# Performance work log

Hardware: AMD Instinct MI355X
Metric: run time of the kernel (lower is better)

Reference implementation:

```python
import math
import jax, jax.numpy as jnp
import numpy as np
from jax import lax

B = 4; N = 4096; F = 15; A = 24          # batch, tcr_num, feature_num, aa_num
HID = 10; H = 1; HD = 10; AFN = 14       # attn hidden, heads, head dim, sum(filter_num)
KS = [2, 3, 4, 5, 6, 7]; FN = [3, 3, 3, 2, 2, 1]
K = int(N * 0.05)                        # routing topk = 204
SCALE = np.float32(1.0 / math.sqrt(HD))


def setup_inputs() -> dict:
    key = jax.random.key(0)
    ks = jax.random.split(key, 24)
    inp = {"x": jax.random.normal(ks[0], (B, N, F, A), jnp.float32)}
    for i, (h, f) in enumerate(zip(KS, FN)):
        inp["conv_w%d" % h] = jax.random.normal(ks[1 + 2 * i], (f, F, h), jnp.float32) * 0.1
        inp["conv_b%d" % h] = jax.random.normal(ks[2 + 2 * i], (f,), jnp.float32) * 0.1
    specs = [("q", HID, AFN), ("k", HID, AFN), ("v", HID, AFN), ("attn", AFN, HID), ("mil", 2, AFN)]
    for j, (nm, o, i_) in enumerate(specs):
        inp["w_" + nm] = jax.random.normal(ks[13 + 2 * j], (o, i_), jnp.float32) * 0.1
        inp["b_" + nm] = jax.random.normal(ks[14 + 2 * j], (o,), jnp.float32) * 0.1
    return inp


def reference(x, conv_w2, conv_b2, conv_w3, conv_b3, conv_w4, conv_b4,
              conv_w5, conv_b5, conv_w6, conv_b6, conv_w7, conv_b7,
              w_q, b_q, w_k, b_k, w_v, b_v, w_attn, b_attn, w_mil, b_mil):
    # --- per-sequence conv feature extraction ---
    xc = x.reshape(-1, F, A)  # [B*N, 15, 24]
    feats = []
    for w, b in [(conv_w2, conv_b2), (conv_w3, conv_b3), (conv_w4, conv_b4),
                 (conv_w5, conv_b5), (conv_w6, conv_b6), (conv_w7, conv_b7)]:
        y = lax.conv_general_dilated(xc, w, (1,), 'VALID',
                                     dimension_numbers=('NCH', 'OIH', 'NCH'))
        y = jax.nn.relu(y + b[None, :, None])
        feats.append(jnp.max(y, axis=-1))  # AdaptiveMaxPool1d(1)
    out = jnp.concatenate(feats, axis=1).reshape(B, N, AFN)  # [B, N, 14]

    # --- QKV projections, split into heads -> [B, H, N, HD] ---
    q = (out @ w_q.T + b_q).reshape(B, N, H, HD).transpose(0, 2, 1, 3)
    k = (out @ w_k.T + b_k).reshape(B, N, H, HD).transpose(0, 2, 1, 3)
    v = (out @ w_v.T + b_v).reshape(B, N, H, HD).transpose(0, 2, 1, 3)

    # --- bi-level routing: full scores, topk over head-mean (detached in torch) ---
    scores_raw = jnp.einsum('bhnd,bhmd->bhnm', q, k)  # [B, H, N, N]
    a_r = jnp.mean(lax.stop_gradient(scores_raw), axis=1)  # [B, N, N]
    _, idx = lax.top_k(a_r, K)  # [B, N, K] int32
    idx_r = jnp.broadcast_to(idx[:, None], (B, H, N, K))

    scores = jnp.take_along_axis(scores_raw * SCALE, idx_r, axis=3)  # [B, H, N, K]
    # gather values per (batch, head, query): v_g[b,h,i,j] = v[b,h,idx[b,h,i,j]]
    v_g = jax.vmap(jax.vmap(lambda vh, ih: vh[ih]))(v, idx_r)  # [B, H, N, K, HD]

    probs = jax.nn.softmax(scores, axis=-1)  # dropout is identity at p=0 / eval
    ctx = jnp.einsum('bhnk,bhnkd->bhnd', probs, v_g)  # [B, H, N, HD]
    ctx = ctx.transpose(0, 2, 1, 3).reshape(B, N, HID)

    ctx = ctx @ w_attn.T + b_attn          # [B, N, 14]
    logits = ctx @ w_mil.T + b_mil          # [B, N, 2]
    pooled = jnp.sum(logits, axis=1) / N    # [B, 2]
    return pooled, probs[:, :, :, None, :]  # probs shaped [B, H, N, 1, K] as in torch
```

## Files before the change

kernel.cpp:

```cpp
#include <hip/hip_runtime.h>
#include <math.h>

#define NB 4
#define NN 4096
#define KSEL 204
#define NBINS 512
#define CANDN 256
#define QKSCALE 0.31622776601683794f

#define WS_Q 0
#define WS_KT (NB * NN * 10)
#define WS_V (2 * NB * NN * 10)
#define WS_LG (3 * NB * NN * 10)

#define SEQ_PER_BLOCK 16


__global__ __launch_bounds__(256) void featqkv_kernel(
    const float* __restrict__ x,
    const float* __restrict__ w2, const float* __restrict__ b2,
    const float* __restrict__ w3, const float* __restrict__ b3,
    const float* __restrict__ w4, const float* __restrict__ b4,
    const float* __restrict__ w5, const float* __restrict__ b5,
    const float* __restrict__ w6, const float* __restrict__ b6,
    const float* __restrict__ w7, const float* __restrict__ b7,
    const float* __restrict__ wq, const float* __restrict__ bq,
    const float* __restrict__ wk, const float* __restrict__ bk,
    const float* __restrict__ wv, const float* __restrict__ bv,
    float* __restrict__ q_out, float* __restrict__ kT_out, float* __restrict__ v_out)
{
    __shared__ __align__(16) float xs[SEQ_PER_BLOCK * 360];
    __shared__ float wpad[14 * 105];
    __shared__ float bconv[14];
    __shared__ float wqkv[420];
    __shared__ float bqkv[30];
    __shared__ float feats[SEQ_PER_BLOCK * 14];

    const int t = threadIdx.x;
    const int g0 = blockIdx.x * SEQ_PER_BLOCK;

    {
        const float4* xg4 = reinterpret_cast<const float4*>(x + (size_t)g0 * 360);
        float4* xs4 = reinterpret_cast<float4*>(xs);
        for (int i = t; i < SEQ_PER_BLOCK * 90; i += 256) xs4[i] = xg4[i];
    }

    for (int i = t; i < 14 * 105; i += 256) {
        const int ch = i / 105;
        const int r = i - ch * 105;
        const int c = r / 7;
        const int j = r - (r / 7) * 7;
        float val = 0.f;
        if (ch < 3)       { if (j < 2) val = w2[ch * 30 + c * 2 + j]; }
        else if (ch < 6)  { if (j < 3) val = w3[(ch - 3) * 45 + c * 3 + j]; }
        else if (ch < 9)  { if (j < 4) val = w4[(ch - 6) * 60 + c * 4 + j]; }
        else if (ch < 11) { if (j < 5) val = w5[(ch - 9) * 75 + c * 5 + j]; }
        else if (ch < 13) { if (j < 6) val = w6[(ch - 11) * 90 + c * 6 + j]; }
        else              { val = w7[c * 7 + j]; }
        wpad[i] = val;
    }
    if (t < 3) bconv[t] = b2[t];
    else if (t < 6) bconv[t] = b3[t - 3];
    else if (t < 9) bconv[t] = b4[t - 6];
    else if (t < 11) bconv[t] = b5[t - 9];
    else if (t < 13) bconv[t] = b6[t - 11];
    else if (t == 13) bconv[t] = b7[0];
    for (int i = t; i < 140; i += 256) wqkv[i] = wq[i];
    for (int i = t; i < 140; i += 256) wqkv[140 + i] = wk[i];
    for (int i = t; i < 140; i += 256) wqkv[280 + i] = wv[i];
    if (t < 10) bqkv[t] = bq[t];
    else if (t < 20) bqkv[t] = bk[t - 10];
    else if (t < 30) bqkv[t] = bv[t - 20];
    __syncthreads();

    const int seq = t >> 4;
    const int wkr = t & 15;

    if (wkr < 14) {
        const int ch = wkr;
        int T;
        if (ch < 3) T = 23; else if (ch < 6) T = 22; else if (ch < 9) T = 21;
        else if (ch < 11) T = 20; else if (ch < 13) T = 19; else T = 18;

        float acc[23];
#pragma unroll
        for (int u = 0; u < 23; u++) acc[u] = 0.f;
        const float* xrow = &xs[seq * 360];
        const float* wrow = &wpad[ch * 105];
        for (int c = 0; c < 15; c++) {
            float xr[30];
            const float4* xp = reinterpret_cast<const float4*>(xrow + c * 24);
#pragma unroll
            for (int u4 = 0; u4 < 6; u4++) {
                const float4 xv = xp[u4];
                xr[u4 * 4 + 0] = xv.x; xr[u4 * 4 + 1] = xv.y;
                xr[u4 * 4 + 2] = xv.z; xr[u4 * 4 + 3] = xv.w;
            }
#pragma unroll
            for (int u = 24; u < 30; u++) xr[u] = 0.f;
#pragma unroll
            for (int j = 0; j < 7; j++) {
                const float wv_ = wrow[c * 7 + j];
#pragma unroll
                for (int tt = 0; tt < 23; tt++)
                    acc[tt] = fmaf(xr[tt + j], wv_, acc[tt]);
            }
        }
        float m = -3.0e38f;
#pragma unroll
        for (int tt = 0; tt < 23; tt++)
            if (tt < T) m = fmaxf(m, acc[tt]);
        feats[seq * 14 + ch] = fmaxf(m + bconv[ch], 0.f);
    }
    __syncthreads();

    const int g = g0 + seq;
    const int b_ = g >> 12;
    const int n_ = g & 4095;
    for (int o = wkr; o < 30; o += 16) {
        const int type = o / 10;
        const int comp = o % 10;
        const float* wrow = &wqkv[type * 140 + comp * 14];
        const float* frow = &feats[seq * 14];
        float a = bqkv[type * 10 + comp];
#pragma unroll
        for (int ii = 0; ii < 14; ii++) a = fmaf(frow[ii], wrow[ii], a);
        if (type == 0) q_out[(size_t)g * 10 + comp] = a;
        else if (type == 1)
            kT_out[(size_t)b_ * 40960 + (size_t)(n_ >> 6) * 640 + comp * 64 + (n_ & 63)] = a;
        else v_out[(size_t)g * 10 + comp] = a;
    }
}

__device__ __forceinline__ float dec_key(unsigned int k) {
    return (k & 0x80000000u) ? __uint_as_float(k ^ 0x80000000u)
                             : __uint_as_float(~k);
}
__device__ __forceinline__ unsigned int enc_key(float s) {
    unsigned int u = __float_as_uint(s);
    return (u & 0x80000000u) ? ~u : (u | 0x80000000u);
}

__global__ __launch_bounds__(256, 8) void attn_kernel(
    const float* __restrict__ qbuf, const float* __restrict__ kTbuf,
    const float* __restrict__ vbuf,
    const float* __restrict__ w_attn, const float* __restrict__ b_attn,
    const float* __restrict__ w_mil, const float* __restrict__ b_mil,
    float* __restrict__ out_probs, float* __restrict__ logits)
{
    __shared__ unsigned int base_[NBINS];
    __shared__ unsigned int bc_[NBINS];
    __shared__ unsigned long long cand[CANDN];
    __shared__ float hpart[4], lpart[4], fpart[4];
    __shared__ unsigned int wtot[4];
    __shared__ float ctxp[40];
    __shared__ float ctx_sh[10];
    __shared__ float attn_sh[14];

    const int t = threadIdx.x;
    const int lane = t & 63;
    const int w = t >> 6;
    const int row = blockIdx.x;
    const int b_ = row >> 12;

    float qr[10];
    {
        const float* qp = qbuf + (size_t)row * 10;
#pragma unroll
        for (int c = 0; c < 10; c++) qr[c] = qp[c];
    }
    const float* kTb = kTbuf + (size_t)b_ * 40960;
    float sc[16];
    float vhi = -1e30f, vlo = 1e30f;
#pragma unroll
    for (int i = 0; i < 4; i++) {
        const float4* kp = reinterpret_cast<const float4*>(
            kTb + (size_t)(i * 16 + (t >> 4)) * 640 + (t & 15) * 4);
        float ax = 0.f, ay = 0.f, az = 0.f, aw = 0.f;
#pragma unroll
        for (int c = 0; c < 10; c++) {
            const float4 kv = kp[c * 16];
            ax = fmaf(qr[c], kv.x, ax);
            ay = fmaf(qr[c], kv.y, ay);
            az = fmaf(qr[c], kv.z, az);
            aw = fmaf(qr[c], kv.w, aw);
        }
        sc[i * 4 + 0] = ax; sc[i * 4 + 1] = ay;
        sc[i * 4 + 2] = az; sc[i * 4 + 3] = aw;
        vhi = fmaxf(vhi, fmaxf(fmaxf(ax, ay), fmaxf(az, aw)));
        vlo = fminf(vlo, fminf(fminf(ax, ay), fminf(az, aw)));
    }
#pragma unroll
    for (int off = 32; off > 0; off >>= 1) {
        vhi = fmaxf(vhi, __shfl_xor(vhi, off));
        vlo = fminf(vlo, __shfl_xor(vlo, off));
    }
    if (lane == 0) { hpart[w] = vhi; lpart[w] = vlo; }
    base_[2 * t] = 0u; base_[2 * t + 1] = 0u;
    cand[t] = 0ULL;
    __syncthreads();
    const float hi = fmaxf(fmaxf(hpart[0], hpart[1]), fmaxf(hpart[2], hpart[3]));
    const float lo = fminf(fminf(lpart[0], lpart[1]), fminf(lpart[2], lpart[3]));
    const bool degen = (hi <= lo);

    float pv = 0.f;
    int jj = 0, p = KSEL;
    bool selected = false;
    const float smax = hi * QKSCALE;

    if (!degen) {
        const float scale = (float)(NBINS - 1) / (hi - lo);

#pragma unroll
        for (int i = 0; i < 16; i++) {
            const int bin = (int)fminf((sc[i] - lo) * scale, (float)(NBINS - 1));
            atomicAdd(&base_[bin], 1u);
        }
        __syncthreads();

        {
            const unsigned int c0 = base_[2 * t];
            const unsigned int c1 = base_[2 * t + 1];
            const unsigned int T_ = c0 + c1;
            unsigned int acc = T_;
#pragma unroll
            for (int off = 1; off < 64; off <<= 1) {
                unsigned int o = __shfl_down(acc, off);
                if (lane + off < 64) acc += o;
            }
            if (lane == 0) wtot[w] = acc;
            __syncthreads();
            unsigned int tail = 0u;
#pragma unroll
            for (int w2 = 1; w2 < 4; w2++) if (w2 > w) tail += wtot[w2];
            const unsigned int A = (acc - T_) + tail;
            base_[2 * t + 1] = A;
            base_[2 * t] = A + c1;
            bc_[2 * t + 1] = A;
            bc_[2 * t] = A + c1;
        }
        __syncthreads();

#pragma unroll
        for (int i = 0; i < 16; i++) {
            const int bin = (int)fminf((sc[i] - lo) * scale, (float)(NBINS - 1));
            const unsigned int bs = base_[bin];
            if (bs < KSEL) {
                const unsigned int pos = atomicAdd(&bc_[bin], 1u);
                if (pos < CANDN) {
                    const int j = (i >> 2) * 1024 + t * 4 + (i & 3);
                    cand[pos] = (((unsigned long long)enc_key(sc[i])) << 16)
                              | (unsigned long long)(4095 - j);
                }
            }
        }
        __syncthreads();

        const unsigned long long mine = cand[t];
        if (mine != 0ULL) {
            const float s = dec_key((unsigned int)(mine >> 16));
            const int bin = (int)fminf((s - lo) * scale, (float)(NBINS - 1));
            const unsigned int bs = base_[bin];
            unsigned int e2 = (bin > 0) ? base_[bin - 1] : 4096u;
            if (e2 > CANDN) e2 = CANDN;
            unsigned int rank = 0;
            for (unsigned int s2 = bs; s2 < e2; s2++)
                rank += (cand[s2] > mine) ? 1u : 0u;
            const unsigned int pp = bs + rank;
            if (pp < KSEL) {
                selected = true;
                p = (int)pp;
                jj = 4095 - (int)(mine & 0xFFFFu);
                pv = expf(s * QKSCALE - smax);
            }
        }
    } else {
        if (t < KSEL) {
            selected = true;
            p = t;
            jj = t;
            pv = 1.f;
        }
    }

    float dsum = pv;
#pragma unroll
    for (int off = 32; off > 0; off >>= 1) dsum += __shfl_xor(dsum, off);
    if (lane == 0) fpart[w] = dsum;
    __syncthreads();
    const float inv = 1.f / (fpart[0] + fpart[1] + fpart[2] + fpart[3]);

    float cx0 = 0.f, cx1 = 0.f, cx2 = 0.f, cx3 = 0.f, cx4 = 0.f;
    float cx5 = 0.f, cx6 = 0.f, cx7 = 0.f, cx8 = 0.f, cx9 = 0.f;
    if (selected) {
        const float pn = pv * inv;
        out_probs[(size_t)row * KSEL + p] = pn;
        const float* vr = vbuf + ((size_t)b_ * NN + (size_t)jj) * 10;
        const float2 v01 = reinterpret_cast<const float2*>(vr)[0];
        const float2 v23 = reinterpret_cast<const float2*>(vr)[1];
        const float2 v45 = reinterpret_cast<const float2*>(vr)[2];
        const float2 v67 = reinterpret_cast<const float2*>(vr)[3];
        const float2 v89 = reinterpret_cast<const float2*>(vr)[4];
        cx0 = pn * v01.x; cx1 = pn * v01.y;
        cx2 = pn * v23.x; cx3 = pn * v23.y;
        cx4 = pn * v45.x; cx5 = pn * v45.y;
        cx6 = pn * v67.x; cx7 = pn * v67.y;
        cx8 = pn * v89.x; cx9 = pn * v89.y;
    }
#pragma unroll
    for (int off = 32; off > 0; off >>= 1) {
        cx0 += __shfl_xor(cx0, off); cx1 += __shfl_xor(cx1, off);
        cx2 += __shfl_xor(cx2, off); cx3 += __shfl_xor(cx3, off);
        cx4 += __shfl_xor(cx4, off); cx5 += __shfl_xor(cx5, off);
        cx6 += __shfl_xor(cx6, off); cx7 += __shfl_xor(cx7, off);
        cx8 += __shfl_xor(cx8, off); cx9 += __shfl_xor(cx9, off);
    }
    if (lane == 0) {
        ctxp[w * 10 + 0] = cx0; ctxp[w * 10 + 1] = cx1; ctxp[w * 10 + 2] = cx2;
        ctxp[w * 10 + 3] = cx3; ctxp[w * 10 + 4] = cx4; ctxp[w * 10 + 5] = cx5;
        ctxp[w * 10 + 6] = cx6; ctxp[w * 10 + 7] = cx7; ctxp[w * 10 + 8] = cx8;
        ctxp[w * 10 + 9] = cx9;
    }
    __syncthreads();
    if (t < 10) ctx_sh[t] = ctxp[t] + ctxp[10 + t] + ctxp[20 + t] + ctxp[30 + t];
    __syncthreads();

    if (t < 14) {
        float a = b_attn[t];
#pragma unroll
        for (int d = 0; d < 10; d++) a = fmaf(ctx_sh[d], w_attn[t * 10 + d], a);
        attn_sh[t] = a;
    }
    __syncthreads();
    if (t < 2) {
        float lg = b_mil[t];
#pragma unroll
        for (int ii = 0; ii < 14; ii++) lg = fmaf(attn_sh[ii], w_mil[t * 14 + ii], lg);
        logits[(size_t)row * 2 + t] = lg;
    }
}

__global__ __launch_bounds__(256) void pool_kernel(
    const float* __restrict__ logits, float* __restrict__ out)
{
    __shared__ float red[256];
    const int t = threadIdx.x;
    const int bc = blockIdx.x;
    const int b_ = bc >> 1;
    const int c_ = bc & 1;
    float a = 0.f;
    for (int n2 = t; n2 < NN; n2 += 256)
        a += logits[((size_t)b_ * NN + n2) * 2 + c_];
    red[t] = a;
    __syncthreads();
    for (int off = 128; off > 0; off >>= 1) {
        if (t < off) red[t] += red[t + off];
        __syncthreads();
    }
    if (t == 0) out[bc] = red[0] * (1.f / 4096.f);
}

extern "C" void kernel_launch(void* const* d_in, const int* in_sizes, int n_in,
                              void* d_out, int out_size, void* d_ws, size_t ws_size,
                              hipStream_t stream) {
    const float* x  = (const float*)d_in[0];
    const float* w2 = (const float*)d_in[1];  const float* b2 = (const float*)d_in[2];
    const float* w3 = (const float*)d_in[3];  const float* b3 = (const float*)d_in[4];
    const float* w4 = (const float*)d_in[5];  const float* b4 = (const float*)d_in[6];
    const float* w5 = (const float*)d_in[7];  const float* b5 = (const float*)d_in[8];
    const float* w6 = (const float*)d_in[9];  const float* b6 = (const float*)d_in[10];
    const float* w7 = (const float*)d_in[11]; const float* b7 = (const float*)d_in[12];
    const float* wq = (const float*)d_in[13]; const float* bq = (const float*)d_in[14];
    const float* wk = (const float*)d_in[15]; const float* bk = (const float*)d_in[16];
    const float* wv = (const float*)d_in[17]; const float* bv = (const float*)d_in[18];
    const float* wat = (const float*)d_in[19]; const float* bat = (const float*)d_in[20];
    const float* wm = (const float*)d_in[21];  const float* bm = (const float*)d_in[22];

    float* ws = (float*)d_ws;
    float* qb = ws + WS_Q;
    float* kT = ws + WS_KT;
    float* vb = ws + WS_V;
    float* lg = ws + WS_LG;
    float* out = (float*)d_out;

    hipLaunchKernelGGL(featqkv_kernel, dim3(NB * NN / SEQ_PER_BLOCK), dim3(256), 0, stream,
                       x, w2, b2, w3, b3, w4, b4, w5, b5, w6, b6, w7, b7,
                       wq, bq, wk, bk, wv, bv, qb, kT, vb);
    hipLaunchKernelGGL(attn_kernel, dim3(NB * NN), dim3(256), 0, stream,
                       qb, kT, vb, wat, bat, wm, bm, out + 8, lg);
    hipLaunchKernelGGL(pool_kernel, dim3(8), dim3(256), 0, stream, lg, out);
}
```

Baseline: 320.1 us.

## Process two query rows per attention block and reuse each K load

Each attention block now handles two adjacent query rows, so every float4 of K is loaded once and used for both rows' dot products. All histogram, scan, candidate and softmax stages are interleaved across the two rows, which halves the grid and the number of barriers per row. K is also stored in a plain [batch, component, n] transposed layout so each thread reads contiguous float4s. In exchange it raises register and shared-memory use per block (launch bound lowered to 4) and gives fewer blocks for latency hiding.

```diff
diff --git a/kernel.cpp b/kernel.cpp
--- a/kernel.cpp
+++ b/kernel.cpp
@@ -126,8 +126,7 @@
 #pragma unroll
         for (int ii = 0; ii < 14; ii++) a = fmaf(frow[ii], wrow[ii], a);
         if (type == 0) q_out[(size_t)g * 10 + comp] = a;
-        else if (type == 1)
-            kT_out[(size_t)b_ * 40960 + (size_t)(n_ >> 6) * 640 + comp * 64 + (n_ & 63)] = a;
+        else if (type == 1) kT_out[((size_t)b_ * 10 + comp) * NN + n_] = a;
         else v_out[(size_t)g * 10 + comp] = a;
     }
 }
@@ -141,202 +140,276 @@
     return (u & 0x80000000u) ? ~u : (u | 0x80000000u);
 }
 
-__global__ __launch_bounds__(256, 8) void attn_kernel(
+__global__ __launch_bounds__(256, 4) void attn_kernel(
     const float* __restrict__ qbuf, const float* __restrict__ kTbuf,
     const float* __restrict__ vbuf,
     const float* __restrict__ w_attn, const float* __restrict__ b_attn,
     const float* __restrict__ w_mil, const float* __restrict__ b_mil,
     float* __restrict__ out_probs, float* __restrict__ logits)
 {
-    __shared__ unsigned int base_[NBINS];
-    __shared__ unsigned int bc_[NBINS];
-    __shared__ unsigned long long cand[CANDN];
-    __shared__ float hpart[4], lpart[4], fpart[4];
-    __shared__ unsigned int wtot[4];
-    __shared__ float ctxp[40];
-    __shared__ float ctx_sh[10];
-    __shared__ float attn_sh[14];
+    __shared__ unsigned int base_[2][NBINS];
+    __shared__ unsigned int bc_[2][NBINS];
+    __shared__ unsigned long long cand[2][CANDN];
+    __shared__ float hpart[2][4], lpart[2][4], fpart[2][4];
+    __shared__ unsigned int wtot[2][4];
+    __shared__ float ctxp[2][40];
+    __shared__ float ctx_sh[2][10];
+    __shared__ float attn_sh[2][14];
 
     const int t = threadIdx.x;
     const int lane = t & 63;
     const int w = t >> 6;
-    const int row = blockIdx.x;
-    const int b_ = row >> 12;
-
-    float qr[10];
+    const int r0 = blockIdx.x * 2;
+    const int b_ = r0 >> 12;
+
+    float qr[2][10];
     {
-        const float* qp = qbuf + (size_t)row * 10;
-#pragma unroll
-        for (int c = 0; c < 10; c++) qr[c] = qp[c];
-    }
-    const float* kTb = kTbuf + (size_t)b_ * 40960;
-    float sc[16];
-    float vhi = -1e30f, vlo = 1e30f;
+        const float4* qp4 = reinterpret_cast<const float4*>(qbuf + (size_t)r0 * 10);
+        const float4 a = qp4[0], b = qp4[1], c = qp4[2], d = qp4[3], e = qp4[4];
+        qr[0][0] = a.x; qr[0][1] = a.y; qr[0][2] = a.z; qr[0][3] = a.w;
+        qr[0][4] = b.x; qr[0][5] = b.y; qr[0][6] = b.z; qr[0][7] = b.w;
+        qr[0][8] = c.x; qr[0][9] = c.y;
+        qr[1][0] = c.z; qr[1][1] = c.w;
+        qr[1][2] = d.x; qr[1][3] = d.y; qr[1][4] = d.z; qr[1][5] = d.w;
+        qr[1][6] = e.x; qr[1][7] = e.y; qr[1][8] = e.z; qr[1][9] = e.w;
+    }
+    const float* kTb = kTbuf + (size_t)b_ * 10 * NN;
+    float sc[2][16];
+    float vhi[2], vlo[2];
+#pragma unroll
+    for (int rr = 0; rr < 2; rr++) { vhi[rr] = -1e30f; vlo[rr] = 1e30f; }
 #pragma unroll
     for (int i = 0; i < 4; i++) {
-        const float4* kp = reinterpret_cast<const float4*>(
-            kTb + (size_t)(i * 16 + (t >> 4)) * 640 + (t & 15) * 4);
-        float ax = 0.f, ay = 0.f, az = 0.f, aw = 0.f;
+        float a0x = 0.f, a0y = 0.f, a0z = 0.f, a0w = 0.f;
+        float a1x = 0.f, a1y = 0.f, a1z = 0.f, a1w = 0.f;
 #pragma unroll
         for (int c = 0; c < 10; c++) {
-            const float4 kv = kp[c * 16];
-            ax = fmaf(qr[c], kv.x, ax);
-            ay = fmaf(qr[c], kv.y, ay);
-            az = fmaf(qr[c], kv.z, az);
-            aw = fmaf(qr[c], kv.w, aw);
-        }
-        sc[i * 4 + 0] = ax; sc[i * 4 + 1] = ay;
-        sc[i * 4 + 2] = az; sc[i * 4 + 3] = aw;
-        vhi = fmaxf(vhi, fmaxf(fmaxf(ax, ay), fmaxf(az, aw)));
-        vlo = fminf(vlo, fminf(fminf(ax, ay), fminf(az, aw)));
+            const float4 kv = reinterpret_cast<const float4*>(kTb + c * NN)[i * 256 + t];
+            a0x = fmaf(qr[0][c], kv.x, a0x);
+            a0y = fmaf(qr[0][c], kv.y, a0y);
+            a0z = fmaf(qr[0][c], kv.z, a0z);
+            a0w = fmaf(qr[0][c], kv.w, a0w);
+            a1x = fmaf(qr[1][c], kv.x, a1x);
+            a1y = fmaf(qr[1][c], kv.y, a1y);
+            a1z = fmaf(qr[1][c], kv.z, a1z);
+            a1w = fmaf(qr[1][c], kv.w, a1w);
+        }
+        sc[0][i * 4 + 0] = a0x; sc[0][i * 4 + 1] = a0y;
+        sc[0][i * 4 + 2] = a0z; sc[0][i * 4 + 3] = a0w;
+        sc[1][i * 4 + 0] = a1x; sc[1][i * 4 + 1] = a1y;
+        sc[1][i * 4 + 2] = a1z; sc[1][i * 4 + 3] = a1w;
+        vhi[0] = fmaxf(vhi[0], fmaxf(fmaxf(a0x, a0y), fmaxf(a0z, a0w)));
+        vlo[0] = fminf(vlo[0], fminf(fminf(a0x, a0y), fminf(a0z, a0w)));
+        vhi[1] = fmaxf(vhi[1], fmaxf(fmaxf(a1x, a1y), fmaxf(a1z, a1w)));
+        vlo[1] = fminf(vlo[1], fminf(fminf(a1x, a1y), fminf(a1z, a1w)));
     }
 #pragma unroll
     for (int off = 32; off > 0; off >>= 1) {
-        vhi = fmaxf(vhi, __shfl_xor(vhi, off));
-        vlo = fminf(vlo, __shfl_xor(vlo, off));
-    }
-    if (lane == 0) { hpart[w] = vhi; lpart[w] = vlo; }
-    base_[2 * t] = 0u; base_[2 * t + 1] = 0u;
-    cand[t] = 0ULL;
-    __syncthreads();
-    const float hi = fmaxf(fmaxf(hpart[0], hpart[1]), fmaxf(hpart[2], hpart[3]));
-    const float lo = fminf(fminf(lpart[0], lpart[1]), fminf(lpart[2], lpart[3]));
-    const bool degen = (hi <= lo);
-
-    float pv = 0.f;
-    int jj = 0, p = KSEL;
-    bool selected = false;
-    const float smax = hi * QKSCALE;
-
-    if (!degen) {
-        const float scale = (float)(NBINS - 1) / (hi - lo);
-
-#pragma unroll
-        for (int i = 0; i < 16; i++) {
-            const int bin = (int)fminf((sc[i] - lo) * scale, (float)(NBINS - 1));
-            atomicAdd(&base_[bin], 1u);
-        }
-        __syncthreads();
-
-        {
-            const unsigned int c0 = base_[2 * t];
-            const unsigned int c1 = base_[2 * t + 1];
-            const unsigned int T_ = c0 + c1;
-            unsigned int acc = T_;
-#pragma unroll
-            for (int off = 1; off < 64; off <<= 1) {
-                unsigned int o = __shfl_down(acc, off);
-                if (lane + off < 64) acc += o;
+#pragma unroll
+        for (int rr = 0; rr < 2; rr++) {
+            vhi[rr] = fmaxf(vhi[rr], __shfl_xor(vhi[rr], off));
+            vlo[rr] = fminf(vlo[rr], __shfl_xor(vlo[rr], off));
+        }
+    }
+    if (lane == 0) {
+#pragma unroll
+        for (int rr = 0; rr < 2; rr++) { hpart[rr][w] = vhi[rr]; lpart[rr][w] = vlo[rr]; }
+    }
+    {
+        unsigned int* bz = &base_[0][0];
+#pragma unroll
+        for (int i = 0; i < 4; i++) bz[t + i * 256] = 0u;
+        unsigned long long* cz = &cand[0][0];
+        cz[t] = 0ULL; cz[t + 256] = 0ULL;
+    }
+    __syncthreads();
+
+    float hi[2], lo[2], scale[2], smax[2];
+    bool degen[2];
+#pragma unroll
+    for (int rr = 0; rr < 2; rr++) {
+        hi[rr] = fmaxf(fmaxf(hpart[rr][0], hpart[rr][1]), fmaxf(hpart[rr][2], hpart[rr][3]));
+        lo[rr] = fminf(fminf(lpart[rr][0], lpart[rr][1]), fminf(lpart[rr][2], lpart[rr][3]));
+        degen[rr] = (hi[rr] <= lo[rr]);
+        scale[rr] = degen[rr] ? 0.f : (float)(NBINS - 1) / (hi[rr] - lo[rr]);
+        smax[rr] = hi[rr] * QKSCALE;
+    }
+
+#pragma unroll
+    for (int rr = 0; rr < 2; rr++) {
+        if (!degen[rr]) {
+#pragma unroll
+            for (int i = 0; i < 16; i++) {
+                const int bin = (int)fminf((sc[rr][i] - lo[rr]) * scale[rr], (float)(NBINS - 1));
+                atomicAdd(&base_[rr][bin], 1u);
             }
-            if (lane == 0) wtot[w] = acc;
-            __syncthreads();
-            unsigned int tail = 0u;
-#pragma unroll
-            for (int w2 = 1; w2 < 4; w2++) if (w2 > w) tail += wtot[w2];
-            const unsigned int A = (acc - T_) + tail;
-            base_[2 * t + 1] = A;
-            base_[2 * t] = A + c1;
-            bc_[2 * t + 1] = A;
-            bc_[2 * t] = A + c1;
-        }
-        __syncthreads();
-
-#pragma unroll
-        for (int i = 0; i < 16; i++) {
-            const int bin = (int)fminf((sc[i] - lo) * scale, (float)(NBINS - 1));
-            const unsigned int bs = base_[bin];
-            if (bs < KSEL) {
-                const unsigned int pos = atomicAdd(&bc_[bin], 1u);
-                if (pos < CANDN) {
-                    const int j = (i >> 2) * 1024 + t * 4 + (i & 3);
-                    cand[pos] = (((unsigned long long)enc_key(sc[i])) << 16)
-                              | (unsigned long long)(4095 - j);
+        }
+    }
+    __syncthreads();
+
+    unsigned int c1s[2], Ts[2], accs[2];
+#pragma unroll
+    for (int rr = 0; rr < 2; rr++) {
+        const unsigned int c0 = base_[rr][2 * t];
+        const unsigned int c1 = base_[rr][2 * t + 1];
+        const unsigned int T_ = c0 + c1;
+        unsigned int acc = T_;
+#pragma unroll
+        for (int off = 1; off < 64; off <<= 1) {
+            unsigned int o = __shfl_down(acc, off);
+            if (lane + off < 64) acc += o;
+        }
+        if (lane == 0) wtot[rr][w] = acc;
+        c1s[rr] = c1; Ts[rr] = T_; accs[rr] = acc;
+    }
+    __syncthreads();
+#pragma unroll
+    for (int rr = 0; rr < 2; rr++) {
+        unsigned int tail = 0u;
+#pragma unroll
+        for (int w2 = 1; w2 < 4; w2++) if (w2 > w) tail += wtot[rr][w2];
+        const unsigned int A = (accs[rr] - Ts[rr]) + tail;
+        base_[rr][2 * t + 1] = A;
+        base_[rr][2 * t] = A + c1s[rr];
+        bc_[rr][2 * t + 1] = A;
+        bc_[rr][2 * t] = A + c1s[rr];
+    }
+    __syncthreads();
+
+#pragma unroll
+    for (int rr = 0; rr < 2; rr++) {
+        if (!degen[rr]) {
+#pragma unroll
+            for (int i = 0; i < 16; i++) {
+                const int bin = (int)fminf((sc[rr][i] - lo[rr]) * scale[rr], (float)(NBINS - 1));
+                const unsigned int bs = base_[rr][bin];
+                if (bs < KSEL) {
+                    const unsigned int pos = atomicAdd(&bc_[rr][bin], 1u);
+                    if (pos < CANDN) {
+                        const int j = (i >> 2) * 1024 + t * 4 + (i & 3);
+                        cand[rr][pos] = (((unsigned long long)enc_key(sc[rr][i])) << 16)
+                                      | (unsigned long long)(4095 - j);
+                    }
                 }
             }
         }
-        __syncthreads();
-
-        const unsigned long long mine = cand[t];
-        if (mine != 0ULL) {
-            const float s = dec_key((unsigned int)(mine >> 16));
-            const int bin = (int)fminf((s - lo) * scale, (float)(NBINS - 1));
-            const unsigned int bs = base_[bin];
-            unsigned int e2 = (bin > 0) ? base_[bin - 1] : 4096u;
-            if (e2 > CANDN) e2 = CANDN;
-            unsigned int rank = 0;
-            for (unsigned int s2 = bs; s2 < e2; s2++)
-                rank += (cand[s2] > mine) ? 1u : 0u;
-            const unsigned int pp = bs + rank;
-            if (pp < KSEL) {
-                selected = true;
-                p = (int)pp;
-                jj = 4095 - (int)(mine & 0xFFFFu);
-                pv = expf(s * QKSCALE - smax);
+    }
+    __syncthreads();
+
+    float pv[2]; int jj[2], p[2]; bool selected[2];
+#pragma unroll
+    for (int rr = 0; rr < 2; rr++) {
+        pv[rr] = 0.f; jj[rr] = 0; p[rr] = KSEL; selected[rr] = false;
+        if (!degen[rr]) {
+            const unsigned long long mine = cand[rr][t];
+            if (mine != 0ULL) {
+                const float s = dec_key((unsigned int)(mine >> 16));
+                const int bin = (int)fminf((s - lo[rr]) * scale[rr], (float)(NBINS - 1));
+                const unsigned int bs = base_[rr][bin];
+                unsigned int e2 = (bin > 0) ? base_[rr][bin - 1] : 4096u;
+                if (e2 > CANDN) e2 = CANDN;
+                unsigned int rank = 0;
+                for (unsigned int s2 = bs; s2 < e2; s2++)
+                    rank += (cand[rr][s2] > mine) ? 1u : 0u;
+                const unsigned int pp = bs + rank;
+                if (pp < KSEL) {
+                    selected[rr] = true;
+                    p[rr] = (int)pp;
+                    jj[rr] = 4095 - (int)(mine & 0xFFFFu);
+                    pv[rr] = expf(s * QKSCALE - smax[rr]);
+                }
             }
-        }
-    } else {
-        if (t < KSEL) {
-            selected = true;
-            p = t;
-            jj = t;
-            pv = 1.f;
-        }
-    }
-
-    float dsum = pv;
-#pragma unroll
-    for (int off = 32; off > 0; off >>= 1) dsum += __shfl_xor(dsum, off);
-    if (lane == 0) fpart[w] = dsum;
-    __syncthreads();
-    const float inv = 1.f / (fpart[0] + fpart[1] + fpart[2] + fpart[3]);
-
-    float cx0 = 0.f, cx1 = 0.f, cx2 = 0.f, cx3 = 0.f, cx4 = 0.f;
-    float cx5 = 0.f, cx6 = 0.f, cx7 = 0.f, cx8 = 0.f, cx9 = 0.f;
-    if (selected) {
-        const float pn = pv * inv;
-        out_probs[(size_t)row * KSEL + p] = pn;
-        const float* vr = vbuf + ((size_t)b_ * NN + (size_t)jj) * 10;
-        const float2 v01 = reinterpret_cast<const float2*>(vr)[0];
-        const float2 v23 = reinterpret_cast<const float2*>(vr)[1];
-        const float2 v45 = reinterpret_cast<const float2*>(vr)[2];
-        const float2 v67 = reinterpret_cast<const float2*>(vr)[3];
-        const float2 v89 = reinterpret_cast<const float2*>(vr)[4];
-        cx0 = pn * v01.x; cx1 = pn * v01.y;
-        cx2 = pn * v23.x; cx3 = pn * v23.y;
-        cx4 = pn * v45.x; cx5 = pn * v45.y;
-        cx6 = pn * v67.x; cx7 = pn * v67.y;
-        cx8 = pn * v89.x; cx9 = pn * v89.y;
-    }
+        } else {
+            if (t < KSEL) { selected[rr] = true; p[rr] = t; jj[rr] = t; pv[rr] = 1.f; }
+        }
+    }
+
+    float dsum[2];
+#pragma unroll
+    for (int rr = 0; rr < 2; rr++) dsum[rr] = pv[rr];
 #pragma unroll
     for (int off = 32; off > 0; off >>= 1) {
-        cx0 += __shfl_xor(cx0, off); cx1 += __shfl_xor(cx1, off);
-        cx2 += __shfl_xor(cx2, off); cx3 += __shfl_xor(cx3, off);
-        cx4 += __shfl_xor(cx4, off); cx5 += __shfl_xor(cx5, off);
-        cx6 += __shfl_xor(cx6, off); cx7 += __shfl_xor(cx7, off);
-        cx8 += __shfl_xor(cx8, off); cx9 += __shfl_xor(cx9, off);
+#pragma unroll
+        for (int rr = 0; rr < 2; rr++) dsum[rr] += __shfl_xor(dsum[rr], off);
     }
     if (lane == 0) {
-        ctxp[w * 10 + 0] = cx0; ctxp[w * 10 + 1] = cx1; ctxp[w * 10 + 2] = cx2;
-        ctxp[w * 10 + 3] = cx3; ctxp[w * 10 + 4] = cx4; ctxp[w * 10 + 5] = cx5;
-        ctxp[w * 10 + 6] = cx6; ctxp[w * 10 + 7] = cx7; ctxp[w * 10 + 8] = cx8;
-        ctxp[w * 10 + 9] = cx9;
-    }
-    __syncthreads();
-    if (t < 10) ctx_sh[t] = ctxp[t] + ctxp[10 + t] + ctxp[20 + t] + ctxp[30 + t];
+#pragma unroll
+        for (int rr = 0; rr < 2; rr++) fpart[rr][w] = dsum[rr];
+    }
+    __syncthreads();
+    float inv[2];
+#pragma unroll
+    for (int rr = 0; rr < 2; rr++)
+        inv[rr] = 1.f / (fpart[rr][0] + fpart[rr][1] + fpart[rr][2] + fpart[rr][3]);
+
+    float cx[2][10];
+#pragma unroll
+    for (int rr = 0; rr < 2; rr++)
+#pragma unroll
+        for (int d = 0; d < 10; d++) cx[rr][d] = 0.f;
+#pragma unroll
+    for (int rr = 0; rr < 2; rr++) {
+        if (selected[rr]) {
+            const float pn = pv[rr] * inv[rr];
+            out_probs[(size_t)(r0 + rr) * KSEL + p[rr]] = pn;
+            const float* vr = vbuf + ((size_t)b_ * NN + (size_t)jj[rr]) * 10;
+            const float2 v01 = reinterpret_cast<const float2*>(vr)[0];
+            const float2 v23 = reinterpret_cast<const float2*>(vr)[1];
+            const float2 v45 = reinterpret_cast<const float2*>(vr)[2];
+            const float2 v67 = reinterpret_cast<const float2*>(vr)[3];
+            const float2 v89 = reinterpret_cast<const float2*>(vr)[4];
+            cx[rr][0] = pn * v01.x; cx[rr][1] = pn * v01.y;
+            cx[rr][2] = pn * v23.x; cx[rr][3] = pn * v23.y;
+            cx[rr][4] = pn * v45.x; cx[rr][5] = pn * v45.y;
+            cx[rr][6] = pn * v67.x; cx[rr][7] = pn * v67.y;
+            cx[rr][8] = pn * v89.x; cx[rr][9] = pn * v89.y;
+        }
+    }
+#pragma unroll
+    for (int off = 32; off > 0; off >>= 1) {
+#pragma unroll
+        for (int rr = 0; rr < 2; rr++)
+#pragma unroll
+            for (int d = 0; d < 10; d++) cx[rr][d] += __shfl_xor(cx[rr][d], off);
+    }
+    if (lane == 0) {
+#pragma unroll
+        for (int rr = 0; rr < 2; rr++)
+#pragma unroll
+            for (int d = 0; d < 10; d++) ctxp[rr][w * 10 + d] = cx[rr][d];
+    }
+    __syncthreads();
+    if (t < 10) ctx_sh[0][t] = ctxp[0][t] + ctxp[0][10 + t] + ctxp[0][20 + t] + ctxp[0][30 + t];
+    else if (t >= 64 && t < 74) {
+        const int d = t - 64;
+        ctx_sh[1][d] = ctxp[1][d] + ctxp[1][10 + d] + ctxp[1][20 + d] + ctxp[1][30 + d];
+    }
     __syncthreads();
 
     if (t < 14) {
         float a = b_attn[t];
 #pragma unroll
-        for (int d = 0; d < 10; d++) a = fmaf(ctx_sh[d], w_attn[t * 10 + d], a);
-        attn_sh[t] = a;
+        for (int d = 0; d < 10; d++) a = fmaf(ctx_sh[0][d], w_attn[t * 10 + d], a);
+        attn_sh[0][t] = a;
+    } else if (t >= 64 && t < 78) {
+        const int o = t - 64;
+        float a = b_attn[o];
+#pragma unroll
+        for (int d = 0; d < 10; d++) a = fmaf(ctx_sh[1][d], w_attn[o * 10 + d], a);
+        attn_sh[1][o] = a;
     }
     __syncthreads();
     if (t < 2) {
         float lg = b_mil[t];
 #pragma unroll
-        for (int ii = 0; ii < 14; ii++) lg = fmaf(attn_sh[ii], w_mil[t * 14 + ii], lg);
-        logits[(size_t)row * 2 + t] = lg;
+        for (int ii = 0; ii < 14; ii++) lg = fmaf(attn_sh[0][ii], w_mil[t * 14 + ii], lg);
+        logits[(size_t)r0 * 2 + t] = lg;
+    } else if (t >= 64 && t < 66) {
+        const int o = t - 64;
+        float lg = b_mil[o];
+#pragma unroll
+        for (int ii = 0; ii < 14; ii++) lg = fmaf(attn_sh[1][ii], w_mil[o * 14 + ii], lg);
+        logits[(size_t)(r0 + 1) * 2 + o] = lg;
     }
 }
 
@@ -386,7 +459,7 @@
     hipLaunchKernelGGL(featqkv_kernel, dim3(NB * NN / SEQ_PER_BLOCK), dim3(256), 0, stream,
                        x, w2, b2, w3, b3, w4, b4, w5, b5, w6, b6, w7, b7,
                        wq, bq, wk, bk, wv, bv, qb, kT, vb);
-    hipLaunchKernelGGL(attn_kernel, dim3(NB * NN), dim3(256), 0, stream,
+    hipLaunchKernelGGL(attn_kernel, dim3(NB * NN / 2), dim3(256), 0, stream,
                        qb, kT, vb, wat, bat, wm, bm, out + 8, lg);
     hipLaunchKernelGGL(pool_kernel, dim3(8), dim3(256), 0, stream, lg, out);
 }
```

Measured after the change: 279.0 us. -12.8%, faster.

## Process one query row per wavefront instead of per block in attention

Applied to the files above, without the earlier changes.

The attention kernel now assigns each query row to a single 64-lane wavefront, with four rows per block. Each wave keeps its own histogram and candidate buffers in shared memory and uses __threadfence_block instead of __syncthreads, so cross-wave barriers and shared partial sums are gone. The K transpose layout changes to a plain [b][comp][n] layout to suit per-wave float4 loads. Each lane now holds 64 scores in registers and does four times the serial histogram and rank work. That raises register pressure and may lower occupancy, while the block-wide reductions for the projection epilogue are removed.

```diff
diff --git a/kernel.cpp b/kernel.cpp
--- a/kernel.cpp
+++ b/kernel.cpp
@@ -126,8 +126,7 @@
 #pragma unroll
         for (int ii = 0; ii < 14; ii++) a = fmaf(frow[ii], wrow[ii], a);
         if (type == 0) q_out[(size_t)g * 10 + comp] = a;
-        else if (type == 1)
-            kT_out[(size_t)b_ * 40960 + (size_t)(n_ >> 6) * 640 + comp * 64 + (n_ & 63)] = a;
+        else if (type == 1) kT_out[((size_t)b_ * 10 + comp) * NN + n_] = a;
         else v_out[(size_t)g * 10 + comp] = a;
     }
 }
@@ -140,53 +139,56 @@
     unsigned int u = __float_as_uint(s);
     return (u & 0x80000000u) ? ~u : (u | 0x80000000u);
 }
-
-__global__ __launch_bounds__(256, 8) void attn_kernel(
+__device__ __forceinline__ int binof(float s, float lo, float scale) {
+    return (int)fminf((s - lo) * scale, (float)(NBINS - 1));
+}
+
+__global__ __launch_bounds__(256) void attn_kernel(
     const float* __restrict__ qbuf, const float* __restrict__ kTbuf,
     const float* __restrict__ vbuf,
     const float* __restrict__ w_attn, const float* __restrict__ b_attn,
     const float* __restrict__ w_mil, const float* __restrict__ b_mil,
     float* __restrict__ out_probs, float* __restrict__ logits)
 {
-    __shared__ unsigned int base_[NBINS];
-    __shared__ unsigned int bc_[NBINS];
-    __shared__ unsigned long long cand[CANDN];
-    __shared__ float hpart[4], lpart[4], fpart[4];
-    __shared__ unsigned int wtot[4];
-    __shared__ float ctxp[40];
-    __shared__ float ctx_sh[10];
-    __shared__ float attn_sh[14];
+    __shared__ unsigned int base_[4][NBINS];
+    __shared__ unsigned int bc_[4][NBINS];
+    __shared__ unsigned long long cand[4][CANDN];
 
     const int t = threadIdx.x;
     const int lane = t & 63;
     const int w = t >> 6;
-    const int row = blockIdx.x;
+    const int row = blockIdx.x * 4 + w;
     const int b_ = row >> 12;
+
+#pragma unroll
+    for (int i = 0; i < 8; i++) base_[w][lane + i * 64] = 0u;
+#pragma unroll
+    for (int i = 0; i < 4; i++) cand[w][lane + i * 64] = 0ULL;
 
     float qr[10];
     {
-        const float* qp = qbuf + (size_t)row * 10;
-#pragma unroll
-        for (int c = 0; c < 10; c++) qr[c] = qp[c];
-    }
-    const float* kTb = kTbuf + (size_t)b_ * 40960;
-    float sc[16];
+        const float2* qp2 = reinterpret_cast<const float2*>(qbuf + (size_t)row * 10);
+        const float2 a = qp2[0], b = qp2[1], c = qp2[2], d = qp2[3], e = qp2[4];
+        qr[0] = a.x; qr[1] = a.y; qr[2] = b.x; qr[3] = b.y; qr[4] = c.x;
+        qr[5] = c.y; qr[6] = d.x; qr[7] = d.y; qr[8] = e.x; qr[9] = e.y;
+    }
+
+    const float* kTb = kTbuf + (size_t)b_ * 10 * NN;
+    float sc[64];
     float vhi = -1e30f, vlo = 1e30f;
 #pragma unroll
-    for (int i = 0; i < 4; i++) {
-        const float4* kp = reinterpret_cast<const float4*>(
-            kTb + (size_t)(i * 16 + (t >> 4)) * 640 + (t & 15) * 4);
+    for (int g = 0; g < 16; g++) {
         float ax = 0.f, ay = 0.f, az = 0.f, aw = 0.f;
 #pragma unroll
         for (int c = 0; c < 10; c++) {
-            const float4 kv = kp[c * 16];
+            const float4 kv = reinterpret_cast<const float4*>(kTb + c * NN)[g * 64 + lane];
             ax = fmaf(qr[c], kv.x, ax);
             ay = fmaf(qr[c], kv.y, ay);
             az = fmaf(qr[c], kv.z, az);
             aw = fmaf(qr[c], kv.w, aw);
         }
-        sc[i * 4 + 0] = ax; sc[i * 4 + 1] = ay;
-        sc[i * 4 + 2] = az; sc[i * 4 + 3] = aw;
+        sc[g * 4 + 0] = ax; sc[g * 4 + 1] = ay;
+        sc[g * 4 + 2] = az; sc[g * 4 + 3] = aw;
         vhi = fmaxf(vhi, fmaxf(fmaxf(ax, ay), fmaxf(az, aw)));
         vlo = fminf(vlo, fminf(fminf(ax, ay), fminf(az, aw)));
     }
@@ -195,148 +197,140 @@
         vhi = fmaxf(vhi, __shfl_xor(vhi, off));
         vlo = fminf(vlo, __shfl_xor(vlo, off));
     }
-    if (lane == 0) { hpart[w] = vhi; lpart[w] = vlo; }
-    base_[2 * t] = 0u; base_[2 * t + 1] = 0u;
-    cand[t] = 0ULL;
-    __syncthreads();
-    const float hi = fmaxf(fmaxf(hpart[0], hpart[1]), fmaxf(hpart[2], hpart[3]));
-    const float lo = fminf(fminf(lpart[0], lpart[1]), fminf(lpart[2], lpart[3]));
+    const float hi = vhi, lo = vlo;
     const bool degen = (hi <= lo);
-
-    float pv = 0.f;
-    int jj = 0, p = KSEL;
-    bool selected = false;
     const float smax = hi * QKSCALE;
+
+    float pv[4]; int pp[4], jj[4]; bool sel[4];
+#pragma unroll
+    for (int q = 0; q < 4; q++) { pv[q] = 0.f; pp[q] = 0; jj[q] = 0; sel[q] = false; }
 
     if (!degen) {
         const float scale = (float)(NBINS - 1) / (hi - lo);
 
 #pragma unroll
-        for (int i = 0; i < 16; i++) {
-            const int bin = (int)fminf((sc[i] - lo) * scale, (float)(NBINS - 1));
-            atomicAdd(&base_[bin], 1u);
-        }
-        __syncthreads();
+        for (int i = 0; i < 64; i++) {
+            const int bin = binof(sc[i], lo, scale);
+            atomicAdd(&base_[w][bin], 1u);
+        }
+        __threadfence_block();
 
         {
-            const unsigned int c0 = base_[2 * t];
-            const unsigned int c1 = base_[2 * t + 1];
-            const unsigned int T_ = c0 + c1;
+            unsigned int c8[8];
+            unsigned int T_ = 0u;
+#pragma unroll
+            for (int k = 0; k < 8; k++) { c8[k] = base_[w][lane * 8 + k]; T_ += c8[k]; }
             unsigned int acc = T_;
 #pragma unroll
             for (int off = 1; off < 64; off <<= 1) {
                 unsigned int o = __shfl_down(acc, off);
                 if (lane + off < 64) acc += o;
             }
-            if (lane == 0) wtot[w] = acc;
-            __syncthreads();
-            unsigned int tail = 0u;
-#pragma unroll
-            for (int w2 = 1; w2 < 4; w2++) if (w2 > w) tail += wtot[w2];
-            const unsigned int A = (acc - T_) + tail;
-            base_[2 * t + 1] = A;
-            base_[2 * t] = A + c1;
-            bc_[2 * t + 1] = A;
-            bc_[2 * t] = A + c1;
-        }
-        __syncthreads();
-
-#pragma unroll
-        for (int i = 0; i < 16; i++) {
-            const int bin = (int)fminf((sc[i] - lo) * scale, (float)(NBINS - 1));
-            const unsigned int bs = base_[bin];
+            unsigned int run = acc - T_;
+#pragma unroll
+            for (int k = 7; k >= 0; k--) {
+                base_[w][lane * 8 + k] = run;
+                bc_[w][lane * 8 + k] = run;
+                run += c8[k];
+            }
+        }
+        __threadfence_block();
+
+#pragma unroll
+        for (int i = 0; i < 64; i++) {
+            const int bin = binof(sc[i], lo, scale);
+            const unsigned int bs = base_[w][bin];
             if (bs < KSEL) {
-                const unsigned int pos = atomicAdd(&bc_[bin], 1u);
+                const unsigned int pos = atomicAdd(&bc_[w][bin], 1u);
                 if (pos < CANDN) {
-                    const int j = (i >> 2) * 1024 + t * 4 + (i & 3);
-                    cand[pos] = (((unsigned long long)enc_key(sc[i])) << 16)
-                              | (unsigned long long)(4095 - j);
+                    const int j = (i >> 2) * 256 + lane * 4 + (i & 3);
+                    cand[w][pos] = (((unsigned long long)enc_key(sc[i])) << 16)
+                                 | (unsigned long long)(4095 - j);
                 }
             }
         }
-        __syncthreads();
-
-        const unsigned long long mine = cand[t];
-        if (mine != 0ULL) {
-            const float s = dec_key((unsigned int)(mine >> 16));
-            const int bin = (int)fminf((s - lo) * scale, (float)(NBINS - 1));
-            const unsigned int bs = base_[bin];
-            unsigned int e2 = (bin > 0) ? base_[bin - 1] : 4096u;
-            if (e2 > CANDN) e2 = CANDN;
-            unsigned int rank = 0;
-            for (unsigned int s2 = bs; s2 < e2; s2++)
-                rank += (cand[s2] > mine) ? 1u : 0u;
-            const unsigned int pp = bs + rank;
-            if (pp < KSEL) {
-                selected = true;
-                p = (int)pp;
-                jj = 4095 - (int)(mine & 0xFFFFu);
-                pv = expf(s * QKSCALE - smax);
+        __threadfence_block();
+
+#pragma unroll
+        for (int q = 0; q < 4; q++) {
+            const int s_idx = lane + 64 * q;
+            const unsigned long long mine = cand[w][s_idx];
+            if (mine != 0ULL) {
+                const float s = dec_key((unsigned int)(mine >> 16));
+                const int bin = binof(s, lo, scale);
+                const unsigned int bs = base_[w][bin];
+                unsigned int e2 = (bin > 0) ? base_[w][bin - 1] : 4096u;
+                if (e2 > CANDN) e2 = CANDN;
+                unsigned int rank = 0;
+                for (unsigned int s2 = bs; s2 < e2; s2++)
+                    rank += (cand[w][s2] > mine) ? 1u : 0u;
+                const unsigned int pq = bs + rank;
+                if (pq < KSEL) {
+                    sel[q] = true;
+                    pp[q] = (int)pq;
+                    jj[q] = 4095 - (int)(mine & 0xFFFFu);
+                    pv[q] = expf(s * QKSCALE - smax);
+                }
             }
         }
     } else {
-        if (t < KSEL) {
-            selected = true;
-            p = t;
-            jj = t;
-            pv = 1.f;
-        }
-    }
-
-    float dsum = pv;
+#pragma unroll
+        for (int q = 0; q < 4; q++) {
+            const int s_idx = lane + 64 * q;
+            if (s_idx < KSEL) { sel[q] = true; pp[q] = s_idx; jj[q] = s_idx; pv[q] = 1.f; }
+        }
+    }
+
+    float dsum = pv[0] + pv[1] + pv[2] + pv[3];
 #pragma unroll
     for (int off = 32; off > 0; off >>= 1) dsum += __shfl_xor(dsum, off);
-    if (lane == 0) fpart[w] = dsum;
-    __syncthreads();
-    const float inv = 1.f / (fpart[0] + fpart[1] + fpart[2] + fpart[3]);
-
-    float cx0 = 0.f, cx1 = 0.f, cx2 = 0.f, cx3 = 0.f, cx4 = 0.f;
-    float cx5 = 0.f, cx6 = 0.f, cx7 = 0.f, cx8 = 0.f, cx9 = 0.f;
-    if (selected) {
-        const float pn = pv * inv;
-        out_probs[(size_t)row * KSEL + p] = pn;
-        const float* vr = vbuf + ((size_t)b_ * NN + (size_t)jj) * 10;
-        const float2 v01 = reinterpret_cast<const float2*>(vr)[0];
-        const float2 v23 = reinterpret_cast<const float2*>(vr)[1];
-        const float2 v45 = reinterpret_cast<const float2*>(vr)[2];
-        const float2 v67 = reinterpret_cast<const float2*>(vr)[3];
-        const float2 v89 = reinterpret_cast<const float2*>(vr)[4];
-        cx0 = pn * v01.x; cx1 = pn * v01.y;
-        cx2 = pn * v23.x; cx3 = pn * v23.y;
-        cx4 = pn * v45.x; cx5 = pn * v45.y;
-        cx6 = pn * v67.x; cx7 = pn * v67.y;
-        cx8 = pn * v89.x; cx9 = pn * v89.y;
+    const float inv = 1.f / dsum;
+
+    float cx[10];
+#pragma unroll
+    for (int d = 0; d < 10; d++) cx[d] = 0.f;
+#pragma unroll
+    for (int q = 0; q < 4; q++) {
+        if (sel[q]) {
+            const float pn = pv[q] * inv;
+            out_probs[(size_t)row * KSEL + pp[q]] = pn;
+            const float* vr = vbuf + ((size_t)b_ * NN + (size_t)jj[q]) * 10;
+            const float2 v01 = reinterpret_cast<const float2*>(vr)[0];
+            const float2 v23 = reinterpret_cast<const float2*>(vr)[1];
+            const float2 v45 = reinterpret_cast<const float2*>(vr)[2];
+            const float2 v67 = reinterpret_cast<const float2*>(vr)[3];
+            const float2 v89 = reinterpret_cast<const float2*>(vr)[4];
+            cx[0] = fmaf(pn, v01.x, cx[0]); cx[1] = fmaf(pn, v01.y, cx[1]);
+            cx[2] = fmaf(pn, v23.x, cx[2]); cx[3] = fmaf(pn, v23.y, cx[3]);
+            cx[4] = fmaf(pn, v45.x, cx[4]); cx[5] = fmaf(pn, v45.y, cx[5]);
+            cx[6] = fmaf(pn, v67.x, cx[6]); cx[7] = fmaf(pn, v67.y, cx[7]);
+            cx[8] = fmaf(pn, v89.x, cx[8]); cx[9] = fmaf(pn, v89.y, cx[9]);
+        }
     }
 #pragma unroll
     for (int off = 32; off > 0; off >>= 1) {
-        cx0 += __shfl_xor(cx0, off); cx1 += __shfl_xor(cx1, off);
-        cx2 += __shfl_xor(cx2, off); cx3 += __shfl_xor(cx3, off);
-        cx4 += __shfl_xor(cx4, off); cx5 += __shfl_xor(cx5, off);
-        cx6 += __shfl_xor(cx6, off); cx7 += __shfl_xor(cx7, off);
-        cx8 += __shfl_xor(cx8, off); cx9 += __shfl_xor(cx9, off);
+#pragma unroll
+        for (int d = 0; d < 10; d++) cx[d] += __shfl_xor(cx[d], off);
+    }
+
+    float m0 = 0.f, m1 = 0.f;
+    if (lane < 14) {
+        float a = b_attn[lane];
+#pragma unroll
+        for (int d = 0; d < 10; d++) a = fmaf(cx[d], w_attn[lane * 10 + d], a);
+        m0 = a * w_mil[lane];
+        m1 = a * w_mil[14 + lane];
+    }
+#pragma unroll
+    for (int off = 8; off > 0; off >>= 1) {
+        m0 += __shfl_xor(m0, off);
+        m1 += __shfl_xor(m1, off);
     }
     if (lane == 0) {
-        ctxp[w * 10 + 0] = cx0; ctxp[w * 10 + 1] = cx1; ctxp[w * 10 + 2] = cx2;
-        ctxp[w * 10 + 3] = cx3; ctxp[w * 10 + 4] = cx4; ctxp[w * 10 + 5] = cx5;
-        ctxp[w * 10 + 6] = cx6; ctxp[w * 10 + 7] = cx7; ctxp[w * 10 + 8] = cx8;
-        ctxp[w * 10 + 9] = cx9;
-    }
-    __syncthreads();
-    if (t < 10) ctx_sh[t] = ctxp[t] + ctxp[10 + t] + ctxp[20 + t] + ctxp[30 + t];
-    __syncthreads();
-
-    if (t < 14) {
-        float a = b_attn[t];
-#pragma unroll
-        for (int d = 0; d < 10; d++) a = fmaf(ctx_sh[d], w_attn[t * 10 + d], a);
-        attn_sh[t] = a;
-    }
-    __syncthreads();
-    if (t < 2) {
-        float lg = b_mil[t];
-#pragma unroll
-        for (int ii = 0; ii < 14; ii++) lg = fmaf(attn_sh[ii], w_mil[t * 14 + ii], lg);
-        logits[(size_t)row * 2 + t] = lg;
+        float2 lgv;
+        lgv.x = m0 + b_mil[0];
+        lgv.y = m1 + b_mil[1];
+        *reinterpret_cast<float2*>(logits + (size_t)row * 2) = lgv;
     }
 }
 
@@ -386,7 +380,7 @@
     hipLaunchKernelGGL(featqkv_kernel, dim3(NB * NN / SEQ_PER_BLOCK), dim3(256), 0, stream,
                        x, w2, b2, w3, b3, w4, b4, w5, b5, w6, b6, w7, b7,
                        wq, bq, wk, bk, wv, bv, qb, kT, vb);
-    hipLaunchKernelGGL(attn_kernel, dim3(NB * NN), dim3(256), 0, stream,
+    hipLaunchKernelGGL(attn_kernel, dim3(NB * NN / 4), dim3(256), 0, stream,
                        qb, kT, vb, wat, bat, wm, bm, out + 8, lg);
     hipLaunchKernelGGL(pool_kernel, dim3(8), dim3(256), 0, stream, lg, out);
 }
```

Result: no change. 316.0 us (-1.3%).
